# Optimization experiments

Measured on AMD Instinct MI355X. Metric: run time of the kernel, lower is better.

The kernel has to match this reference:

```python
import jax, jax.numpy as jnp
import numpy as np

N, D, O, V, E, C = 100000, 128, 128, 3, 400000, 2

def setup_inputs() -> dict:
    key = jax.random.key(0)
    ks = jax.random.split(key, 32)
    s = 0.05
    inp = {
        'features': jax.random.normal(ks[0], (N, D), jnp.float32),
        'edge_index': jax.random.randint(ks[1], (V, 2, E), 0, N, jnp.int32),
        'edge_weight': jax.random.uniform(ks[2], (V, E), jnp.float32),
        # per-view RelationAggregator (single relation each)
        'rel_w': jax.random.normal(ks[3], (V, D, O)) * s,
        'rel_b': jnp.zeros((V, O)),
        'gate_w': jax.random.normal(ks[4], (V, O, O)) * s,
        'gate_b': jnp.zeros((V, O)),
        # LabelAwareAttention
        'la_w1': jax.random.normal(ks[5], (C, D, D // 2)) * s,
        'la_b1': jnp.zeros((C, D // 2)),
        'la_w2': jax.random.normal(ks[6], (C, D // 2)) * s,
        'la_b2': jnp.zeros((C,)),
        'pred_w': jax.random.normal(ks[7], (D, C)) * s,
        'pred_b': jnp.zeros((C,)),
        'att_bias': jnp.float32(0.1),
        # ViewLevelAttention
        'view_pref': jax.random.normal(ks[8], (V, O)),
        'va_w1': jax.random.normal(ks[9], (O, O // 2)) * s,
        'va_b1': jnp.zeros((O // 2,)),
        'va_w2': jax.random.normal(ks[10], (O // 2,)) * s,
        'va_b2': jnp.float32(0.0),
        # linear heads
        'ft_w': jax.random.normal(ks[11], (D, O)) * s,
        'ft_b': jnp.zeros((O,)),
        'sl_w': jax.random.normal(ks[12], (D, O)) * s,
        'sl_b': jnp.zeros((O,)),
        'fus_w': jax.random.normal(ks[13], (2 * O, O)) * s,
        'fus_b': jnp.zeros((O,)),
        'ln_g': jnp.ones((O,)),
        'ln_beta': jnp.zeros((O,)),
    }
    return inp


def _aggregate_view(features, ei, ew, w, b, gw, gb):
    # gather -> linear -> edge weight -> scatter-add (fused segment_sum)
    msg = (features[ei[0]] @ w + b) * ew[:, None]          # [E, O]
    agg = jax.ops.segment_sum(msg, ei[1], num_segments=N)  # [N, O]
    # relation_weight_net: softmax over 1 relation == 1.0 (identity)
    gate = jax.nn.sigmoid(agg @ gw + gb)
    return gate * agg


def reference(features, edge_index, edge_weight, rel_w, rel_b, gate_w, gate_b,
              la_w1, la_b1, la_w2, la_b2, pred_w, pred_b, att_bias,
              view_pref, va_w1, va_b1, va_w2, va_b2,
              ft_w, ft_b, sl_w, sl_b, fus_w, fus_b, ln_g, ln_beta):
    # --- label-aware attention ---
    class_probs = jax.nn.softmax(features @ pred_w + pred_b, axis=-1)        # [N, C]
    h = jax.nn.relu(jnp.einsum('nd,cdk->nck', features, la_w1) + la_b1)      # [N, C, D/2]
    scores = jax.nn.sigmoid(jnp.einsum('nck,ck->nc', h, la_w2) + la_b2)      # [N, C]
    node_att = jnp.sum(scores * class_probs, axis=-1) + att_bias             # [N]

    # --- per-view relation aggregation ---
    views = jax.vmap(_aggregate_view, in_axes=(None, 0, 0, 0, 0, 0, 0))(
        features, edge_index, edge_weight, rel_w, rel_b, gate_w, gate_b)     # [V, N, O]

    # --- view-level attention ---
    pe = views * view_pref[:, None, :]                                       # [V, N, O]
    vh = jax.nn.relu(jnp.einsum('vno,ok->vnk', pe, va_w1) + va_b1)           # [V, N, O/2]
    vscore = jnp.einsum('vnk,k->vn', vh, va_w2) + va_b2                      # [V, N]
    v_att = jax.nn.softmax(vscore, axis=0)                                   # over views
    combined = jnp.sum(views * v_att[..., None], axis=0)                     # [N, O]

    # --- fusion (dropout in eval mode == identity) ---
    self_out = features @ sl_w + sl_b
    transformed = features @ ft_w + ft_b
    weighted = combined * node_att[:, None]
    fused = jax.nn.relu(jnp.concatenate([self_out, weighted], axis=-1) @ fus_w + fus_b)
    out = fused + transformed

    mu = jnp.mean(out, axis=-1, keepdims=True)
    var = jnp.mean(jnp.square(out - mu), axis=-1, keepdims=True)
    out = (out - mu) / jnp.sqrt(var + 1e-5) * ln_g + ln_beta
    return out, class_probs
```

## Files before the change

### kernel.cpp

```cpp
#include <hip/hip_runtime.h>

#define N_ 100000
#define D_ 128
#define O_ 128
#define V_ 3
#define E_ 400000
#define NB_SCAN 98
#define EGRID 1563
#define MB 32
#define NBLK (N_ / MB)
#define LDA 136

typedef unsigned short u16;
typedef __attribute__((ext_vector_type(8))) short bf16x8;
typedef __attribute__((ext_vector_type(4))) float f32x4;

#define MFMA16x16x32 __builtin_amdgcn_mfma_f32_16x16x32_bf16

#define P_RELB  0
#define P_GATEB 384
#define P_VP    768
#define P_VAB1  1152
#define P_VAW2  1216
#define P_VAB2  1280
#define P_LAB1  1281
#define P_LAW2  1409
#define P_LAB2  1537
#define P_PREDB 1539
#define P_ATTB  1541
#define P_FTB   1542
#define P_LNG   1670
#define P_LNB   1798
#define P_PREDW 1926
#define P_TOTAL 2182

__device__ __forceinline__ float b2f(u16 u) {
    union { float f; unsigned int i; } x; x.i = ((unsigned int)u) << 16; return x.f;
}
__device__ __forceinline__ u16 f2b(float f) {
    union { float f; unsigned int i; } x; x.f = f;
    unsigned int r = x.i + 0x7FFFu + ((x.i >> 16) & 1u);
    return (u16)(r >> 16);
}

template<int F32> __device__ __forceinline__ float LD(const void* p, size_t i) {
    if (F32) return ((const float*)p)[i];
    return b2f(((const u16*)p)[i]);
}

__global__ void k_detect(const u16* __restrict__ feat, int* __restrict__ flag) {
    if (threadIdx.x == 0 && blockIdx.x == 0) {
        int bad = 0, zeros = 0;
        for (int i = 0; i < 128; ++i) {
            u16 u = feat[2 * i];
            if (u == 0) zeros++;
            float v = b2f(u);
            if (!(v > -128.f && v < 128.f)) bad++;
        }
        flag[0] = (bad >= 16 || zeros >= 64) ? 1 : 0;
    }
}

template<int F32>
__device__ __forceinline__ void cvt_body(const void* feat, u16* __restrict__ featB) {
    size_t idx = (size_t)blockIdx.x * 256 + threadIdx.x;
    if (F32) {
        const float4* fp = (const float4*)feat;
        float4 a = fp[idx * 2], b = fp[idx * 2 + 1];
        uint4 u;
        u.x = (unsigned)f2b(a.x) | ((unsigned)f2b(a.y) << 16);
        u.y = (unsigned)f2b(a.z) | ((unsigned)f2b(a.w) << 16);
        u.z = (unsigned)f2b(b.x) | ((unsigned)f2b(b.y) << 16);
        u.w = (unsigned)f2b(b.z) | ((unsigned)f2b(b.w) << 16);
        ((uint4*)featB)[idx] = u;
    } else {
        ((uint4*)featB)[idx] = ((const uint4*)feat)[idx];
    }
}
__global__ __launch_bounds__(256) void k_cvt(const int* __restrict__ flag,
                                             const void* feat, u16* __restrict__ featB) {
    if (flag[0]) cvt_body<1>(feat, featB); else cvt_body<0>(feat, featB);
}

template<int F32>
__device__ __forceinline__ void prew_body(const void* sl_w, const void* sl_b,
                                          const void* fus_w, const void* fus_b,
                                          u16* __restrict__ W1T, float* __restrict__ b1) {
    int gid = blockIdx.x * 256 + threadIdx.x;
    int d = gid >> 7, o = gid & 127;
    float acc = 0.f;
    for (int k = 0; k < 128; ++k)
        acc += LD<F32>(sl_w, d * 128 + k) * LD<F32>(fus_w, k * 128 + o);
    W1T[o * 128 + d] = f2b(acc);
    if (gid < 128) {
        float accb = 0.f;
        for (int k = 0; k < 128; ++k)
            accb += LD<F32>(sl_b, k) * LD<F32>(fus_w, k * 128 + gid);
        b1[gid] = accb + LD<F32>(fus_b, gid);
    }
}
__global__ __launch_bounds__(256) void k_prew(const int* __restrict__ flag,
                                              const void* sl_w, const void* sl_b,
                                              const void* fus_w, const void* fus_b,
                                              u16* __restrict__ W1T, float* __restrict__ b1) {
    if (flag[0]) prew_body<1>(sl_w, sl_b, fus_w, fus_b, W1T, b1);
    else         prew_body<0>(sl_w, sl_b, fus_w, fus_b, W1T, b1);
}

template<int F32>
__device__ __forceinline__ void prep_body(
        const void* rel_w, const void* gate_w, const void* va_w1, const void* fus_w,
        const void* ft_w, const void* la_w1,
        const void* rel_b, const void* gate_b, const void* vpref,
        const void* va_b1, const void* va_w2, const void* va_b2,
        const void* la_b1, const void* la_w2, const void* la_b2,
        const void* pred_b, const void* att_bias, const void* ft_b,
        const void* ln_g, const void* ln_beta, const void* pred_w,
        u16* __restrict__ relT, u16* __restrict__ gateT, u16* __restrict__ vaT,
        u16* __restrict__ fus2T, u16* __restrict__ ftT, u16* __restrict__ laT,
        float* __restrict__ P) {
    int id = blockIdx.x * 256 + threadIdx.x;
    if (id < 49152) {
        int v = id >> 14, r = id & 16383, o = r >> 7, d = r & 127;
        relT[id] = f2b(LD<F32>(rel_w, (size_t)v * 16384 + d * 128 + o));
    } else if (id < 98304) {
        int t = id - 49152, v = t >> 14, r = t & 16383, o = r >> 7, d = r & 127;
        gateT[t] = f2b(LD<F32>(gate_w, (size_t)v * 16384 + d * 128 + o));
    } else if (id < 106496) {
        int t = id - 98304, n = t >> 7, k = t & 127;
        vaT[t] = f2b(LD<F32>(va_w1, k * 64 + n));
    } else if (id < 122880) {
        int t = id - 106496, n = t >> 7, k = t & 127;
        fus2T[t] = f2b(LD<F32>(fus_w, (128 + k) * 128 + n));
    } else if (id < 139264) {
        int t = id - 122880, o = t >> 7, d = t & 127;
        ftT[t] = f2b(LD<F32>(ft_w, d * 128 + o));
    } else if (id < 155648) {
        int t = id - 139264, n = t >> 7, d = t & 127;
        int c = n >> 6, j = n & 63;
        laT[t] = f2b(LD<F32>(la_w1, c * 8192 + d * 64 + j));
    } else if (id < 155648 + P_TOTAL) {
        int t = id - 155648;
        float val;
        if      (t < P_GATEB) val = LD<F32>(rel_b, t);
        else if (t < P_VP)    val = LD<F32>(gate_b, t - P_GATEB);
        else if (t < P_VAB1)  val = LD<F32>(vpref, t - P_VP);
        else if (t < P_VAW2)  val = LD<F32>(va_b1, t - P_VAB1);
        else if (t < P_VAB2)  val = LD<F32>(va_w2, t - P_VAW2);
        else if (t < P_LAB1)  val = LD<F32>(va_b2, 0);
        else if (t < P_LAW2)  val = LD<F32>(la_b1, t - P_LAB1);
        else if (t < P_LAB2)  val = LD<F32>(la_w2, t - P_LAW2);
        else if (t < P_PREDB) val = LD<F32>(la_b2, t - P_LAB2);
        else if (t < P_ATTB)  val = LD<F32>(pred_b, t - P_PREDB);
        else if (t < P_FTB)   val = LD<F32>(att_bias, 0);
        else if (t < P_LNG)   val = LD<F32>(ft_b, t - P_FTB);
        else if (t < P_LNB)   val = LD<F32>(ln_g, t - P_LNG);
        else if (t < P_PREDW) val = LD<F32>(ln_beta, t - P_LNB);
        else                  val = LD<F32>(pred_w, t - P_PREDW);
        P[t] = val;
    }
}
__global__ __launch_bounds__(256) void k_prep(const int* __restrict__ flag,
        const void* rel_w, const void* gate_w, const void* va_w1, const void* fus_w,
        const void* ft_w, const void* la_w1,
        const void* rel_b, const void* gate_b, const void* vpref,
        const void* va_b1, const void* va_w2, const void* va_b2,
        const void* la_b1, const void* la_w2, const void* la_b2,
        const void* pred_b, const void* att_bias, const void* ft_b,
        const void* ln_g, const void* ln_beta, const void* pred_w,
        u16* __restrict__ relT, u16* __restrict__ gateT, u16* __restrict__ vaT,
        u16* __restrict__ fus2T, u16* __restrict__ ftT, u16* __restrict__ laT,
        float* __restrict__ P) {
    if (flag[0]) prep_body<1>(rel_w, gate_w, va_w1, fus_w, ft_w, la_w1,
                              rel_b, gate_b, vpref, va_b1, va_w2, va_b2,
                              la_b1, la_w2, la_b2, pred_b, att_bias, ft_b,
                              ln_g, ln_beta, pred_w, relT, gateT, vaT, fus2T, ftT, laT, P);
    else         prep_body<0>(rel_w, gate_w, va_w1, fus_w, ft_w, la_w1,
                              rel_b, gate_b, vpref, va_b1, va_w2, va_b2,
                              la_b1, la_w2, la_b2, pred_b, att_bias, ft_b,
                              ln_g, ln_beta, pred_w, relT, gateT, vaT, fus2T, ftT, laT, P);
}

__global__ __launch_bounds__(256) void k_count(const int* __restrict__ ei,
                                               int* __restrict__ cur3) {
    int v = blockIdx.x / EGRID;
    int e = (blockIdx.x % EGRID) * 256 + threadIdx.x;
    if (e < E_) atomicAdd(&cur3[v * N_ + ei[(size_t)v * 2 * E_ + E_ + e]], 1);
}

__global__ __launch_bounds__(256) void k_scan_bsum(const int* __restrict__ cur3,
                                                   int* __restrict__ bsum) {
    __shared__ int red[256];
    const int v = blockIdx.x / NB_SCAN, b = blockIdx.x % NB_SCAN, tid = threadIdx.x;
    const int base = b * 1024;
    const int* counts = cur3 + v * N_;
    int s = 0;
    for (int i = tid; i < 1024; i += 256) {
        int idx = base + i;
        s += (idx < N_) ? counts[idx] : 0;
    }
    red[tid] = s;
    __syncthreads();
    for (int st = 128; st >= 1; st >>= 1) {
        if (tid < st) red[tid] += red[tid + st];
        __syncthreads();
    }
    if (tid == 0) bsum[v * 128 + b] = red[0];
}

__global__ __launch_bounds__(256) void k_scan_write(int* __restrict__ cur3,
                                                    const int* __restrict__ bsum,
                                                    int* __restrict__ offs3) {
    __shared__ int lsum[256];
    __shared__ int bs_s[128];
    const int v = blockIdx.x / NB_SCAN, b = blockIdx.x % NB_SCAN, tid = threadIdx.x;
    const int base = b * 1024;
    int* counts = cur3 + v * N_;
    int* offs   = offs3 + v * N_;
    if (tid < 128) bs_s[tid] = (tid < b) ? bsum[v * 128 + tid] : 0;
    int c[4]; int s = 0;
    #pragma unroll
    for (int k = 0; k < 4; ++k) {
        int idx = base + tid * 4 + k;
        c[k] = (idx < N_) ? counts[idx] : 0;
        s += c[k];
    }
    lsum[tid] = s;
    __syncthreads();
    for (int st = 1; st < 256; st <<= 1) {
        int t = (tid >= st) ? lsum[tid - st] : 0;
        __syncthreads();
        lsum[tid] += t;
        __syncthreads();
    }
    for (int st = 64; st >= 1; st >>= 1) {
        if (tid < st) bs_s[tid] += bs_s[tid + st];
        __syncthreads();
    }
    int off = bs_s[0] + lsum[tid] - s;
    #pragma unroll
    for (int k = 0; k < 4; ++k) {
        int idx = base + tid * 4 + k;
        if (idx < N_) { offs[idx] = off; counts[idx] = off; }
        off += c[k];
    }
}

template<int F32>
__device__ __forceinline__ void place_body(const int* __restrict__ ei, const void* ew_all,
                                           int* __restrict__ cur3, int2* __restrict__ srcw3) {
    int v = blockIdx.x / EGRID;
    int e = (blockIdx.x % EGRID) * 256 + threadIdx.x;
    if (e < E_) {
        int dst = ei[(size_t)v * 2 * E_ + E_ + e];
        int src = ei[(size_t)v * 2 * E_ + e];
        float w = LD<F32>(ew_all, (size_t)v * E_ + e);
        int pos = atomicAdd(&cur3[v * N_ + dst], 1);
        int2 sw; sw.x = src; sw.y = __float_as_int(w);
        srcw3[(size_t)v * E_ + pos] = sw;
    }
}
__global__ __launch_bounds__(256) void k_place(const int* __restrict__ flag,
                                               const int* __restrict__ ei, const void* ew,
                                               int* __restrict__ cur3, int2* __restrict__ srcw3) {
    if (flag[0]) place_body<1>(ei, ew, cur3, srcw3);
    else         place_body<0>(ei, ew, cur3, srcw3);
}

__global__ __launch_bounds__(256, 4) void k_fused(const int* __restrict__ flag,
        const u16* __restrict__ featB, const int2* __restrict__ srcw3,
        const int* __restrict__ offs3, const int* __restrict__ ends3,
        const u16* __restrict__ relT, const u16* __restrict__ gateT,
        const u16* __restrict__ vaT, const u16* __restrict__ W1T,
        const u16* __restrict__ fus2T, const u16* __restrict__ ftT,
        const u16* __restrict__ laT,
        const float* __restrict__ b1, const float* __restrict__ P,
        void* __restrict__ d_out) {
    const int f32 = flag[0];

    __shared__ __align__(16) u16 xA[MB * LDA];
    __shared__ __align__(16) u16 zb[2][MB * LDA];
    __shared__ float wsn_s[2][MB];
    __shared__ float vsc_s[MB][3];
    __shared__ float red_s[4][MB][2];
    __shared__ float mrs_s[MB][2];
    __shared__ float aw_s[MB][3];
    __shared__ float natt_s[MB];
    __shared__ float lg_s[MB][2];
    __shared__ float relb_s[2][128];
    __shared__ float gateb_s[128], vp_s[128];
    __shared__ float vab1_s[64], vaw2_s[64];
    __shared__ float lab1_s[128], law2_s[128], predw_s[256];
    __shared__ float b1_s[128], ftb_s[128], lng_s[128], lnb_s[128];

    const int tid = threadIdx.x;
    const int wid = tid >> 6;
    const int L = tid & 63, q = L >> 4, i = L & 15;
    const int nb = wid * 32;
    const int nodebase = blockIdx.x * MB;
    const int nl = tid >> 5, l32 = tid & 31, o4 = l32 * 4;
    const f32x4 zz = {0.f, 0.f, 0.f, 0.f};

    auto ldf = [&](const u16* B, int row, int k0) -> bf16x8 {
        return *(const bf16x8*)&B[row * LDA + k0];
    };
    auto ldg = [&](const u16* B, int row, int k0) -> bf16x8 {
        return *(const bf16x8*)&B[row * 128 + k0];
    };
    auto gemm128 = [&](const u16* A, const u16* Bg, f32x4 acc[2][2]) {
        #pragma unroll
        for (int kk = 0; kk < 4; ++kk) {
            int k0 = q * 8 + kk * 32;
            bf16x8 a0 = ldf(A, i, k0);
            bf16x8 a1 = ldf(A, i + 16, k0);
            bf16x8 bb0 = ldg(Bg, nb + i, k0);
            bf16x8 bb1 = ldg(Bg, nb + 16 + i, k0);
            acc[0][0] = MFMA16x16x32(a0, bb0, acc[0][0], 0, 0, 0);
            acc[0][1] = MFMA16x16x32(a0, bb1, acc[0][1], 0, 0, 0);
            acc[1][0] = MFMA16x16x32(a1, bb0, acc[1][0], 0, 0, 0);
            acc[1][1] = MFMA16x16x32(a1, bb1, acc[1][1], 0, 0, 0);
        }
    };
    auto gather = [&](int v, u16* dst) {
        const int* offs = offs3 + v * N_;
        const int* ends = ends3 + v * N_;
        const int2* srcw = srcw3 + (size_t)v * E_;
        int js[4], je[4];
        #pragma unroll
        for (int rep = 0; rep < 4; ++rep) {
            int node = nodebase + rep * 8 + nl;
            js[rep] = offs[node];
            je[rep] = ends[node];
        }
        #pragma unroll
        for (int rep = 0; rep < 4; ++rep) {
            int m = rep * 8 + nl;
            float z0 = 0.f, z1 = 0.f, z2 = 0.f, z3 = 0.f, ws = 0.f;
            int j = js[rep], jend = je[rep];
            for (; j + 3 < jend; j += 4) {
                int2 e0 = srcw[j], e1 = srcw[j + 1], e2 = srcw[j + 2], e3 = srcw[j + 3];
                float w0 = __int_as_float(e0.y), w1 = __int_as_float(e1.y);
                float w2 = __int_as_float(e2.y), w3 = __int_as_float(e3.y);
                ushort4 x0 = *(const ushort4*)&featB[(size_t)e0.x * 128 + o4];
                ushort4 x1 = *(const ushort4*)&featB[(size_t)e1.x * 128 + o4];
                ushort4 x2 = *(const ushort4*)&featB[(size_t)e2.x * 128 + o4];
                ushort4 x3 = *(const ushort4*)&featB[(size_t)e3.x * 128 + o4];
                z0 += w0 * b2f(x0.x) + w1 * b2f(x1.x) + w2 * b2f(x2.x) + w3 * b2f(x3.x);
                z1 += w0 * b2f(x0.y) + w1 * b2f(x1.y) + w2 * b2f(x2.y) + w3 * b2f(x3.y);
                z2 += w0 * b2f(x0.z) + w1 * b2f(x1.z) + w2 * b2f(x2.z) + w3 * b2f(x3.z);
                z3 += w0 * b2f(x0.w) + w1 * b2f(x1.w) + w2 * b2f(x2.w) + w3 * b2f(x3.w);
                ws += w0 + w1 + w2 + w3;
            }
            if (j + 1 < jend) {
                int2 e0 = srcw[j], e1 = srcw[j + 1];
                float w0 = __int_as_float(e0.y), w1 = __int_as_float(e1.y);
                ushort4 x0 = *(const ushort4*)&featB[(size_t)e0.x * 128 + o4];
                ushort4 x1 = *(const ushort4*)&featB[(size_t)e1.x * 128 + o4];
                z0 += w0 * b2f(x0.x) + w1 * b2f(x1.x);
                z1 += w0 * b2f(x0.y) + w1 * b2f(x1.y);
                z2 += w0 * b2f(x0.z) + w1 * b2f(x1.z);
                z3 += w0 * b2f(x0.w) + w1 * b2f(x1.w);
                ws += w0 + w1;
                j += 2;
            }
            if (j < jend) {
                int2 e0 = srcw[j];
                float w0 = __int_as_float(e0.y);
                ushort4 x0 = *(const ushort4*)&featB[(size_t)e0.x * 128 + o4];
                z0 += w0 * b2f(x0.x); z1 += w0 * b2f(x0.y);
                z2 += w0 * b2f(x0.z); z3 += w0 * b2f(x0.w);
                ws += w0;
            }
            uint2 u;
            u.x = (unsigned)f2b(z0) | ((unsigned)f2b(z1) << 16);
            u.y = (unsigned)f2b(z2) | ((unsigned)f2b(z3) << 16);
            *(uint2*)&dst[m * LDA + o4] = u;
            if (l32 == 0) wsn_s[v & 1][m] = ws;
        }
    };

    for (int idx = tid; idx < MB * 16; idx += 256) {
        int m = idx >> 4, s = idx & 15;
        *(uint4*)&xA[m * LDA + s * 8] =
            *(const uint4*)&featB[(size_t)(nodebase + m) * 128 + s * 8];
    }
    if (tid < 64) { vab1_s[tid] = P[P_VAB1 + tid]; vaw2_s[tid] = P[P_VAW2 + tid]; }
    if (tid < 128) {
        b1_s[tid]   = b1[tid];
        ftb_s[tid]  = P[P_FTB + tid];
        lng_s[tid]  = P[P_LNG + tid];
        lnb_s[tid]  = P[P_LNB + tid];
        relb_s[0][tid] = P[P_RELB + tid];
        lab1_s[tid] = P[P_LAB1 + tid];
        law2_s[tid] = P[P_LAW2 + tid];
    }
    predw_s[tid] = P[P_PREDW + tid];
    gather(0, zb[0]);
    __syncthreads();

    f32x4 accL[2][2] = {{zz, zz}, {zz, zz}};
    gemm128(xA, laT, accL);
    #pragma unroll
    for (int rep = 0; rep < 4; ++rep) {
        int m = rep * 8 + nl;
        float lg0 = 0.f, lg1 = 0.f;
        #pragma unroll
        for (int t = 0; t < 4; ++t) {
            float xv = b2f(xA[m * LDA + o4 + t]);
            lg0 += xv * predw_s[(o4 + t) * 2 + 0];
            lg1 += xv * predw_s[(o4 + t) * 2 + 1];
        }
        #pragma unroll
        for (int s = 1; s <= 16; s <<= 1) {
            lg0 += __shfl_xor(lg0, s);
            lg1 += __shfl_xor(lg1, s);
        }
        if (l32 == 0) { lg_s[m][0] = lg0; lg_s[m][1] = lg1; }
    }
    {
        float partL[2][4];
        #pragma unroll
        for (int mt = 0; mt < 2; ++mt)
            #pragma unroll
            for (int r = 0; r < 4; ++r) {
                float h0 = fmaxf(accL[mt][0][r] + lab1_s[nb + i], 0.f);
                float h1 = fmaxf(accL[mt][1][r] + lab1_s[nb + 16 + i], 0.f);
                partL[mt][r] = h0 * law2_s[nb + i] + h1 * law2_s[nb + 16 + i];
            }
        #pragma unroll
        for (int s = 1; s <= 8; s <<= 1)
            #pragma unroll
            for (int mt = 0; mt < 2; ++mt)
                #pragma unroll
                for (int r = 0; r < 4; ++r)
                    partL[mt][r] += __shfl_xor(partL[mt][r], s);
        if (i == 0)
            #pragma unroll
            for (int mt = 0; mt < 2; ++mt)
                #pragma unroll
                for (int r = 0; r < 4; ++r)
                    red_s[wid][mt * 16 + q * 4 + r][0] = partL[mt][r];
    }
    __syncthreads();
    if (tid < MB) {
        float c0 = red_s[0][tid][0] + red_s[1][tid][0] + P[P_LAB2 + 0];
        float c1 = red_s[2][tid][0] + red_s[3][tid][0] + P[P_LAB2 + 1];
        float s0 = 1.f / (1.f + __expf(-c0));
        float s1 = 1.f / (1.f + __expf(-c1));
        float l0 = lg_s[tid][0] + P[P_PREDB + 0];
        float l1 = lg_s[tid][1] + P[P_PREDB + 1];
        float mx = fmaxf(l0, l1);
        float e0 = __expf(l0 - mx), e1 = __expf(l1 - mx);
        float inv = 1.f / (e0 + e1);
        float p0 = e0 * inv, p1 = e1 * inv;
        natt_s[tid] = s0 * p0 + s1 * p1 + P[P_ATTB];
        int node = nodebase + tid;
        if (f32) {
            float* pr = (float*)d_out + (size_t)N_ * O_;
            pr[node * 2 + 0] = p0; pr[node * 2 + 1] = p1;
        } else {
            u16* pr = (u16*)d_out + (size_t)N_ * O_;
            pr[node * 2 + 0] = f2b(p0); pr[node * 2 + 1] = f2b(p1);
        }
    }

    f32x4 viewr[3][2][2];
    #pragma unroll
    for (int v = 0; v < 3; ++v) {
        u16* zc = zb[v & 1];
        f32x4 accA[2][2] = {{zz, zz}, {zz, zz}};
        gemm128(zc, relT + (size_t)v * 16384, accA);
        if (v < 2) {
            if (tid < 128) relb_s[(v + 1) & 1][tid] = P[P_RELB + (v + 1) * 128 + tid];
            gather(v + 1, zb[(v + 1) & 1]);
        }
        if (tid < 128) {
            gateb_s[tid] = P[P_GATEB + v * 128 + tid];
            vp_s[tid]    = P[P_VP + v * 128 + tid];
        }
        __syncthreads();
        #pragma unroll
        for (int mt = 0; mt < 2; ++mt)
            #pragma unroll
            for (int nt = 0; nt < 2; ++nt)
                #pragma unroll
                for (int r = 0; r < 4; ++r) {
                    int row = mt * 16 + q * 4 + r, col = nb + nt * 16 + i;
                    float a = accA[mt][nt][r] + wsn_s[v & 1][row] * relb_s[v & 1][col];
                    accA[mt][nt][r] = a;
                    zc[row * LDA + col] = f2b(a);
                }
        __syncthreads();
        f32x4 acc2[2][2] = {{zz, zz}, {zz, zz}};
        gemm128(zc, gateT + (size_t)v * 16384, acc2);
        __syncthreads();
        #pragma unroll
        for (int mt = 0; mt < 2; ++mt)
            #pragma unroll
            for (int nt = 0; nt < 2; ++nt)
                #pragma unroll
                for (int r = 0; r < 4; ++r) {
                    int row = mt * 16 + q * 4 + r, col = nb + nt * 16 + i;
                    float g = 1.f / (1.f + __expf(-(acc2[mt][nt][r] + gateb_s[col])));
                    float vv = g * accA[mt][nt][r];
                    viewr[v][mt][nt][r] = vv;
                    zc[row * LDA + col] = f2b(vv * vp_s[col]);
                }
        __syncthreads();
        f32x4 accV[2] = {zz, zz};
        const int nbv = wid * 16, colv = nbv + i;
        #pragma unroll
        for (int kk = 0; kk < 4; ++kk) {
            int k0 = q * 8 + kk * 32;
            bf16x8 a0 = ldf(zc, i, k0);
            bf16x8 a1 = ldf(zc, i + 16, k0);
            bf16x8 bb = ldg(vaT, nbv + i, k0);
            accV[0] = MFMA16x16x32(a0, bb, accV[0], 0, 0, 0);
            accV[1] = MFMA16x16x32(a1, bb, accV[1], 0, 0, 0);
        }
        float part[2][4];
        #pragma unroll
        for (int mt = 0; mt < 2; ++mt)
            #pragma unroll
            for (int r = 0; r < 4; ++r) {
                float vh = fmaxf(accV[mt][r] + vab1_s[colv], 0.f);
                part[mt][r] = vh * vaw2_s[colv];
            }
        #pragma unroll
        for (int s = 1; s <= 8; s <<= 1)
            #pragma unroll
            for (int mt = 0; mt < 2; ++mt)
                #pragma unroll
                for (int r = 0; r < 4; ++r)
                    part[mt][r] += __shfl_xor(part[mt][r], s);
        if (i == 0)
            #pragma unroll
            for (int mt = 0; mt < 2; ++mt)
                #pragma unroll
                for (int r = 0; r < 4; ++r)
                    red_s[wid][mt * 16 + q * 4 + r][0] = part[mt][r];
        __syncthreads();
        if (tid < MB)
            vsc_s[tid][v] = red_s[0][tid][0] + red_s[1][tid][0] +
                            red_s[2][tid][0] + red_s[3][tid][0] + P[P_VAB2];
    }

    if (tid < MB) {
        float s0 = vsc_s[tid][0], s1 = vsc_s[tid][1], s2 = vsc_s[tid][2];
        float mx = fmaxf(s0, fmaxf(s1, s2));
        float e0 = __expf(s0 - mx), e1 = __expf(s1 - mx), e2 = __expf(s2 - mx);
        float inv = natt_s[tid] / (e0 + e1 + e2);
        aw_s[tid][0] = e0 * inv; aw_s[tid][1] = e1 * inv; aw_s[tid][2] = e2 * inv;
    }
    __syncthreads();
    u16* wt = zb[0];
    #pragma unroll
    for (int mt = 0; mt < 2; ++mt)
        #pragma unroll
        for (int nt = 0; nt < 2; ++nt)
            #pragma unroll
            for (int r = 0; r < 4; ++r) {
                int row = mt * 16 + q * 4 + r, col = nb + nt * 16 + i;
                float wv = aw_s[row][0] * viewr[0][mt][nt][r] +
                           aw_s[row][1] * viewr[1][mt][nt][r] +
                           aw_s[row][2] * viewr[2][mt][nt][r];
                wt[row * LDA + col] = f2b(wv);
            }
    f32x4 accF[2][2] = {{zz, zz}, {zz, zz}};
    gemm128(xA, W1T, accF);
    __syncthreads();
    gemm128(wt, fus2T, accF);
    float fR[2][2][4];
    #pragma unroll
    for (int mt = 0; mt < 2; ++mt)
        #pragma unroll
        for (int nt = 0; nt < 2; ++nt)
            #pragma unroll
            for (int r = 0; r < 4; ++r) {
                int col = nb + nt * 16 + i;
                fR[mt][nt][r] = fmaxf(accF[mt][nt][r] + b1_s[col], 0.f);
            }
    f32x4 accT[2][2] = {{zz, zz}, {zz, zz}};
    gemm128(xA, ftT, accT);

    float ov[2][2][4], ps[2][4], pq[2][4];
    #pragma unroll
    for (int mt = 0; mt < 2; ++mt)
        #pragma unroll
        for (int r = 0; r < 4; ++r) { ps[mt][r] = 0.f; pq[mt][r] = 0.f; }
    #pragma unroll
    for (int mt = 0; mt < 2; ++mt)
        #pragma unroll
        for (int nt = 0; nt < 2; ++nt)
            #pragma unroll
            for (int r = 0; r < 4; ++r) {
                int col = nb + nt * 16 + i;
                float o = fR[mt][nt][r] + accT[mt][nt][r] + ftb_s[col];
                ov[mt][nt][r] = o;
                ps[mt][r] += o; pq[mt][r] += o * o;
            }
    #pragma unroll
    for (int s = 1; s <= 8; s <<= 1)
        #pragma unroll
        for (int mt = 0; mt < 2; ++mt)
            #pragma unroll
            for (int r = 0; r < 4; ++r) {
                ps[mt][r] += __shfl_xor(ps[mt][r], s);
                pq[mt][r] += __shfl_xor(pq[mt][r], s);
            }
    if (i == 0)
        #pragma unroll
        for (int mt = 0; mt < 2; ++mt)
            #pragma unroll
            for (int r = 0; r < 4; ++r) {
                red_s[wid][mt * 16 + q * 4 + r][0] = ps[mt][r];
                red_s[wid][mt * 16 + q * 4 + r][1] = pq[mt][r];
            }
    __syncthreads();
    if (tid < MB) {
        float sm = red_s[0][tid][0] + red_s[1][tid][0] + red_s[2][tid][0] + red_s[3][tid][0];
        float sq = red_s[0][tid][1] + red_s[1][tid][1] + red_s[2][tid][1] + red_s[3][tid][1];
        float mu = sm * (1.f / 128.f);
        float var = sq * (1.f / 128.f) - mu * mu;
        mrs_s[tid][0] = mu; mrs_s[tid][1] = rsqrtf(var + 1e-5f);
    }
    __syncthreads();
    float* outf = (float*)zb;
    u16*   outb = (u16*)zb;
    #pragma unroll
    for (int mt = 0; mt < 2; ++mt)
        #pragma unroll
        for (int nt = 0; nt < 2; ++nt)
            #pragma unroll
            for (int r = 0; r < 4; ++r) {
                int row = mt * 16 + q * 4 + r, col = nb + nt * 16 + i;
                float val = (ov[mt][nt][r] - mrs_s[row][0]) * mrs_s[row][1]
                            * lng_s[col] + lnb_s[col];
                if (f32) outf[row * 128 + col] = val;
                else     outb[row * 128 + col] = f2b(val);
            }
    __syncthreads();
    if (f32) {
        float* op = (float*)d_out + (size_t)nodebase * 128;
        for (int idx = tid; idx < 1024; idx += 256)
            ((float4*)op)[idx] = ((const float4*)outf)[idx];
    } else {
        u16* op = (u16*)d_out + (size_t)nodebase * 128;
        for (int idx = tid; idx < 512; idx += 256)
            ((uint4*)op)[idx] = ((const uint4*)outb)[idx];
    }
}

extern "C" void kernel_launch(void* const* d_in, const int* in_sizes, int n_in,
                              void* d_out, int out_size, void* d_ws, size_t ws_size,
                              hipStream_t stream) {
    const void* feat     = d_in[0];
    const int*  ei       = (const int*)d_in[1];
    const void* ew       = d_in[2];
    const void* rel_w    = d_in[3];
    const void* rel_b    = d_in[4];
    const void* gate_w   = d_in[5];
    const void* gate_b   = d_in[6];
    const void* la_w1    = d_in[7];
    const void* la_b1    = d_in[8];
    const void* la_w2    = d_in[9];
    const void* la_b2    = d_in[10];
    const void* pred_w   = d_in[11];
    const void* pred_b   = d_in[12];
    const void* att_bias = d_in[13];
    const void* view_pref= d_in[14];
    const void* va_w1    = d_in[15];
    const void* va_b1    = d_in[16];
    const void* va_w2    = d_in[17];
    const void* va_b2    = d_in[18];
    const void* ft_w     = d_in[19];
    const void* ft_b     = d_in[20];
    const void* sl_w     = d_in[21];
    const void* sl_b     = d_in[22];
    const void* fus_w    = d_in[23];
    const void* fus_b    = d_in[24];
    const void* ln_g     = d_in[25];
    const void* ln_beta  = d_in[26];

    int*   flag  = (int*)d_ws;
    int*   offs3 = flag + 4;
    int*   cur3  = offs3 + 3 * N_;
    int2*  srcw3 = (int2*)(cur3 + 3 * N_);
    int*   bsum  = (int*)(srcw3 + 3 * E_);
    float* b1    = (float*)(bsum + 3 * 128);
    float* P     = b1 + 128;
    u16*   W1T   = (u16*)(P + 2304);
    u16*   relT  = W1T + 16384;
    u16*   gateT = relT + 3 * 16384;
    u16*   vaT   = gateT + 3 * 16384;
    u16*   fus2T = vaT + 8192;
    u16*   ftT   = fus2T + 16384;
    u16*   laT   = ftT + 16384;
    u16*   featB = laT + 16384;

    k_detect<<<1, 64, 0, stream>>>((const u16*)feat, flag);
    k_cvt<<<6250, 256, 0, stream>>>(flag, feat, featB);
    k_prew<<<64, 256, 0, stream>>>(flag, sl_w, sl_b, fus_w, fus_b, W1T, b1);
    k_prep<<<617, 256, 0, stream>>>(flag, rel_w, gate_w, va_w1, fus_w, ft_w, la_w1,
                                    rel_b, gate_b, view_pref, va_b1, va_w2, va_b2,
                                    la_b1, la_w2, la_b2, pred_b, att_bias, ft_b,
                                    ln_g, ln_beta, pred_w,
                                    relT, gateT, vaT, fus2T, ftT, laT, P);
    (void)hipMemsetAsync(cur3, 0, 3 * N_ * sizeof(int), stream);
    k_count<<<3 * EGRID, 256, 0, stream>>>(ei, cur3);
    k_scan_bsum<<<3 * NB_SCAN, 256, 0, stream>>>(cur3, bsum);
    k_scan_write<<<3 * NB_SCAN, 256, 0, stream>>>(cur3, bsum, offs3);
    k_place<<<3 * EGRID, 256, 0, stream>>>(flag, ei, ew, cur3, srcw3);
    k_fused<<<NBLK, 256, 0, stream>>>(flag, featB, srcw3, offs3, cur3,
                                      relT, gateT, vaT, W1T, fus2T, ftT, laT,
                                      b1, P, d_out);
}
```

Baseline: 566.5 us.

## Merge prep kernels into one launch, halve node tile, widen gather vectors

The conversion, weight precompute, weight prep and edge-count kernels are merged into a single multi-role launch, and the bf16 feature copy is skipped when inputs are already bf16. The fused node kernel now processes 16 nodes per block instead of 32, with launch bounds raised to 8 blocks per CU. Each node's gather is handled by 16 lanes doing 8-wide loads in place of 32 lanes doing 4-wide loads. The detect kernel uses a warp shuffle reduction instead of a serial loop. Together these aim to cut launch overhead and improve occupancy and latency hiding in the gather, at the cost of less MFMA reuse per block and more blocks overall.

```diff
diff --git a/kernel.cpp b/kernel.cpp
--- a/kernel.cpp
+++ b/kernel.cpp
@@ -7,9 +7,14 @@
 #define E_ 400000
 #define NB_SCAN 98
 #define EGRID 1563
-#define MB 32
+#define MB 16
 #define NBLK (N_ / MB)
 #define LDA 136
+
+#define PRE_CVT  6250
+#define PRE_PREW (PRE_CVT + 64)
+#define PRE_PREP (PRE_PREW + 617)
+#define PRE_TOT  (PRE_PREP + 3 * EGRID)
 
 typedef unsigned short u16;
 typedef __attribute__((ext_vector_type(8))) short bf16x8;
@@ -37,6 +42,12 @@
 __device__ __forceinline__ float b2f(u16 u) {
     union { float f; unsigned int i; } x; x.i = ((unsigned int)u) << 16; return x.f;
 }
+__device__ __forceinline__ float blo(unsigned int u) {
+    union { float f; unsigned int i; } x; x.i = u << 16; return x.f;
+}
+__device__ __forceinline__ float bhi(unsigned int u) {
+    union { float f; unsigned int i; } x; x.i = u & 0xffff0000u; return x.f;
+}
 __device__ __forceinline__ u16 f2b(float f) {
     union { float f; unsigned int i; } x; x.f = f;
     unsigned int r = x.i + 0x7FFFu + ((x.i >> 16) & 1u);
@@ -49,44 +60,38 @@
 }
 
 __global__ void k_detect(const u16* __restrict__ feat, int* __restrict__ flag) {
-    if (threadIdx.x == 0 && blockIdx.x == 0) {
-        int bad = 0, zeros = 0;
-        for (int i = 0; i < 128; ++i) {
-            u16 u = feat[2 * i];
-            if (u == 0) zeros++;
-            float v = b2f(u);
-            if (!(v > -128.f && v < 128.f)) bad++;
-        }
-        flag[0] = (bad >= 16 || zeros >= 64) ? 1 : 0;
-    }
+    int t = threadIdx.x;
+    u16 a = feat[2 * t], b = feat[2 * t + 128];
+    int zeros = (a == 0 ? 1 : 0) + (b == 0 ? 1 : 0);
+    float va = b2f(a), vb = b2f(b);
+    int bad = (!(va > -128.f && va < 128.f) ? 1 : 0) +
+              (!(vb > -128.f && vb < 128.f) ? 1 : 0);
+    #pragma unroll
+    for (int s = 1; s <= 32; s <<= 1) {
+        bad += __shfl_xor(bad, s);
+        zeros += __shfl_xor(zeros, s);
+    }
+    if (t == 0) flag[0] = (bad >= 16 || zeros >= 64) ? 1 : 0;
+}
+
+__device__ __forceinline__ void cvt_body_f32(int b, const void* feat,
+                                             u16* __restrict__ featB) {
+    size_t idx = (size_t)b * 256 + threadIdx.x;
+    const float4* fp = (const float4*)feat;
+    float4 a = fp[idx * 2], c = fp[idx * 2 + 1];
+    uint4 u;
+    u.x = (unsigned)f2b(a.x) | ((unsigned)f2b(a.y) << 16);
+    u.y = (unsigned)f2b(a.z) | ((unsigned)f2b(a.w) << 16);
+    u.z = (unsigned)f2b(c.x) | ((unsigned)f2b(c.y) << 16);
+    u.w = (unsigned)f2b(c.z) | ((unsigned)f2b(c.w) << 16);
+    ((uint4*)featB)[idx] = u;
 }
 
 template<int F32>
-__device__ __forceinline__ void cvt_body(const void* feat, u16* __restrict__ featB) {
-    size_t idx = (size_t)blockIdx.x * 256 + threadIdx.x;
-    if (F32) {
-        const float4* fp = (const float4*)feat;
-        float4 a = fp[idx * 2], b = fp[idx * 2 + 1];
-        uint4 u;
-        u.x = (unsigned)f2b(a.x) | ((unsigned)f2b(a.y) << 16);
-        u.y = (unsigned)f2b(a.z) | ((unsigned)f2b(a.w) << 16);
-        u.z = (unsigned)f2b(b.x) | ((unsigned)f2b(b.y) << 16);
-        u.w = (unsigned)f2b(b.z) | ((unsigned)f2b(b.w) << 16);
-        ((uint4*)featB)[idx] = u;
-    } else {
-        ((uint4*)featB)[idx] = ((const uint4*)feat)[idx];
-    }
-}
-__global__ __launch_bounds__(256) void k_cvt(const int* __restrict__ flag,
-                                             const void* feat, u16* __restrict__ featB) {
-    if (flag[0]) cvt_body<1>(feat, featB); else cvt_body<0>(feat, featB);
-}
-
-template<int F32>
-__device__ __forceinline__ void prew_body(const void* sl_w, const void* sl_b,
+__device__ __forceinline__ void prew_body(int b, const void* sl_w, const void* sl_b,
                                           const void* fus_w, const void* fus_b,
                                           u16* __restrict__ W1T, float* __restrict__ b1) {
-    int gid = blockIdx.x * 256 + threadIdx.x;
+    int gid = b * 256 + threadIdx.x;
     int d = gid >> 7, o = gid & 127;
     float acc = 0.f;
     for (int k = 0; k < 128; ++k)
@@ -99,16 +104,9 @@
         b1[gid] = accb + LD<F32>(fus_b, gid);
     }
 }
-__global__ __launch_bounds__(256) void k_prew(const int* __restrict__ flag,
-                                              const void* sl_w, const void* sl_b,
-                                              const void* fus_w, const void* fus_b,
-                                              u16* __restrict__ W1T, float* __restrict__ b1) {
-    if (flag[0]) prew_body<1>(sl_w, sl_b, fus_w, fus_b, W1T, b1);
-    else         prew_body<0>(sl_w, sl_b, fus_w, fus_b, W1T, b1);
-}
 
 template<int F32>
-__device__ __forceinline__ void prep_body(
+__device__ __forceinline__ void prep_body(int b,
         const void* rel_w, const void* gate_w, const void* va_w1, const void* fus_w,
         const void* ft_w, const void* la_w1,
         const void* rel_b, const void* gate_b, const void* vpref,
@@ -119,7 +117,7 @@
         u16* __restrict__ relT, u16* __restrict__ gateT, u16* __restrict__ vaT,
         u16* __restrict__ fus2T, u16* __restrict__ ftT, u16* __restrict__ laT,
         float* __restrict__ P) {
-    int id = blockIdx.x * 256 + threadIdx.x;
+    int id = b * 256 + threadIdx.x;
     if (id < 49152) {
         int v = id >> 14, r = id & 16383, o = r >> 7, d = r & 127;
         relT[id] = f2b(LD<F32>(rel_w, (size_t)v * 16384 + d * 128 + o));
@@ -160,8 +158,12 @@
         P[t] = val;
     }
 }
-__global__ __launch_bounds__(256) void k_prep(const int* __restrict__ flag,
-        const void* rel_w, const void* gate_w, const void* va_w1, const void* fus_w,
+
+__global__ __launch_bounds__(256) void k_preC(const int* __restrict__ flag,
+        const void* feat, u16* __restrict__ featB,
+        const void* sl_w, const void* sl_b, const void* fus_w, const void* fus_b,
+        u16* __restrict__ W1T, float* __restrict__ b1,
+        const void* rel_w, const void* gate_w, const void* va_w1,
         const void* ft_w, const void* la_w1,
         const void* rel_b, const void* gate_b, const void* vpref,
         const void* va_b1, const void* va_w2, const void* va_b2,
@@ -170,22 +172,29 @@
         const void* ln_g, const void* ln_beta, const void* pred_w,
         u16* __restrict__ relT, u16* __restrict__ gateT, u16* __restrict__ vaT,
         u16* __restrict__ fus2T, u16* __restrict__ ftT, u16* __restrict__ laT,
-        float* __restrict__ P) {
-    if (flag[0]) prep_body<1>(rel_w, gate_w, va_w1, fus_w, ft_w, la_w1,
-                              rel_b, gate_b, vpref, va_b1, va_w2, va_b2,
-                              la_b1, la_w2, la_b2, pred_b, att_bias, ft_b,
-                              ln_g, ln_beta, pred_w, relT, gateT, vaT, fus2T, ftT, laT, P);
-    else         prep_body<0>(rel_w, gate_w, va_w1, fus_w, ft_w, la_w1,
-                              rel_b, gate_b, vpref, va_b1, va_w2, va_b2,
-                              la_b1, la_w2, la_b2, pred_b, att_bias, ft_b,
-                              ln_g, ln_beta, pred_w, relT, gateT, vaT, fus2T, ftT, laT, P);
-}
-
-__global__ __launch_bounds__(256) void k_count(const int* __restrict__ ei,
-                                               int* __restrict__ cur3) {
-    int v = blockIdx.x / EGRID;
-    int e = (blockIdx.x % EGRID) * 256 + threadIdx.x;
-    if (e < E_) atomicAdd(&cur3[v * N_ + ei[(size_t)v * 2 * E_ + E_ + e]], 1);
+        float* __restrict__ P,
+        const int* __restrict__ ei, int* __restrict__ cur3) {
+    int b = blockIdx.x;
+    if (b < PRE_CVT) {
+        if (flag[0]) cvt_body_f32(b, feat, featB);
+    } else if (b < PRE_PREW) {
+        if (flag[0]) prew_body<1>(b - PRE_CVT, sl_w, sl_b, fus_w, fus_b, W1T, b1);
+        else         prew_body<0>(b - PRE_CVT, sl_w, sl_b, fus_w, fus_b, W1T, b1);
+    } else if (b < PRE_PREP) {
+        if (flag[0]) prep_body<1>(b - PRE_PREW, rel_w, gate_w, va_w1, fus_w, ft_w, la_w1,
+                                  rel_b, gate_b, vpref, va_b1, va_w2, va_b2,
+                                  la_b1, la_w2, la_b2, pred_b, att_bias, ft_b,
+                                  ln_g, ln_beta, pred_w, relT, gateT, vaT, fus2T, ftT, laT, P);
+        else         prep_body<0>(b - PRE_PREW, rel_w, gate_w, va_w1, fus_w, ft_w, la_w1,
+                                  rel_b, gate_b, vpref, va_b1, va_w2, va_b2,
+                                  la_b1, la_w2, la_b2, pred_b, att_bias, ft_b,
+                                  ln_g, ln_beta, pred_w, relT, gateT, vaT, fus2T, ftT, laT, P);
+    } else {
+        int b2 = b - PRE_PREP;
+        int v = b2 / EGRID;
+        int e = (b2 % EGRID) * 256 + threadIdx.x;
+        if (e < E_) atomicAdd(&cur3[v * N_ + ei[(size_t)v * 2 * E_ + E_ + e]], 1);
+    }
 }
 
 __global__ __launch_bounds__(256) void k_scan_bsum(const int* __restrict__ cur3,
@@ -267,8 +276,9 @@
     else         place_body<0>(ei, ew, cur3, srcw3);
 }
 
-__global__ __launch_bounds__(256, 4) void k_fused(const int* __restrict__ flag,
-        const u16* __restrict__ featB, const int2* __restrict__ srcw3,
+__global__ __launch_bounds__(256, 8) void k_fused(const int* __restrict__ flag,
+        const void* feat, const u16* __restrict__ featB_,
+        const int2* __restrict__ srcw3,
         const int* __restrict__ offs3, const int* __restrict__ ends3,
         const u16* __restrict__ relT, const u16* __restrict__ gateT,
         const u16* __restrict__ vaT, const u16* __restrict__ W1T,
@@ -277,6 +287,7 @@
         const float* __restrict__ b1, const float* __restrict__ P,
         void* __restrict__ d_out) {
     const int f32 = flag[0];
+    const u16* __restrict__ fb = f32 ? featB_ : (const u16*)feat;
 
     __shared__ __align__(16) u16 xA[MB * LDA];
     __shared__ __align__(16) u16 zb[2][MB * LDA];
@@ -287,10 +298,8 @@
     __shared__ float aw_s[MB][3];
     __shared__ float natt_s[MB];
     __shared__ float lg_s[MB][2];
-    __shared__ float relb_s[2][128];
-    __shared__ float gateb_s[128], vp_s[128];
     __shared__ float vab1_s[64], vaw2_s[64];
-    __shared__ float lab1_s[128], law2_s[128], predw_s[256];
+    __shared__ float predw_s[256];
     __shared__ float b1_s[128], ftb_s[128], lng_s[128], lnb_s[128];
 
     const int tid = threadIdx.x;
@@ -299,6 +308,7 @@
     const int nb = wid * 32;
     const int nodebase = blockIdx.x * MB;
     const int nl = tid >> 5, l32 = tid & 31, o4 = l32 * 4;
+    const int gg = tid >> 4, l16 = tid & 15, o8 = l16 * 8;
     const f32x4 zz = {0.f, 0.f, 0.f, 0.f};
 
     auto ldf = [&](const u16* B, int row, int k0) -> bf16x8 {
@@ -307,101 +317,83 @@
     auto ldg = [&](const u16* B, int row, int k0) -> bf16x8 {
         return *(const bf16x8*)&B[row * 128 + k0];
     };
-    auto gemm128 = [&](const u16* A, const u16* Bg, f32x4 acc[2][2]) {
+    auto gemm128 = [&](const u16* A, const u16* Bg, f32x4 acc[2]) {
         #pragma unroll
         for (int kk = 0; kk < 4; ++kk) {
             int k0 = q * 8 + kk * 32;
             bf16x8 a0 = ldf(A, i, k0);
-            bf16x8 a1 = ldf(A, i + 16, k0);
             bf16x8 bb0 = ldg(Bg, nb + i, k0);
             bf16x8 bb1 = ldg(Bg, nb + 16 + i, k0);
-            acc[0][0] = MFMA16x16x32(a0, bb0, acc[0][0], 0, 0, 0);
-            acc[0][1] = MFMA16x16x32(a0, bb1, acc[0][1], 0, 0, 0);
-            acc[1][0] = MFMA16x16x32(a1, bb0, acc[1][0], 0, 0, 0);
-            acc[1][1] = MFMA16x16x32(a1, bb1, acc[1][1], 0, 0, 0);
+            acc[0] = MFMA16x16x32(a0, bb0, acc[0], 0, 0, 0);
+            acc[1] = MFMA16x16x32(a0, bb1, acc[1], 0, 0, 0);
         }
     };
     auto gather = [&](int v, u16* dst) {
         const int* offs = offs3 + v * N_;
         const int* ends = ends3 + v * N_;
         const int2* srcw = srcw3 + (size_t)v * E_;
-        int js[4], je[4];
-        #pragma unroll
-        for (int rep = 0; rep < 4; ++rep) {
-            int node = nodebase + rep * 8 + nl;
-            js[rep] = offs[node];
-            je[rep] = ends[node];
-        }
-        #pragma unroll
-        for (int rep = 0; rep < 4; ++rep) {
-            int m = rep * 8 + nl;
-            float z0 = 0.f, z1 = 0.f, z2 = 0.f, z3 = 0.f, ws = 0.f;
-            int j = js[rep], jend = je[rep];
-            for (; j + 3 < jend; j += 4) {
-                int2 e0 = srcw[j], e1 = srcw[j + 1], e2 = srcw[j + 2], e3 = srcw[j + 3];
-                float w0 = __int_as_float(e0.y), w1 = __int_as_float(e1.y);
-                float w2 = __int_as_float(e2.y), w3 = __int_as_float(e3.y);
-                ushort4 x0 = *(const ushort4*)&featB[(size_t)e0.x * 128 + o4];
-                ushort4 x1 = *(const ushort4*)&featB[(size_t)e1.x * 128 + o4];
-                ushort4 x2 = *(const ushort4*)&featB[(size_t)e2.x * 128 + o4];
-                ushort4 x3 = *(const ushort4*)&featB[(size_t)e3.x * 128 + o4];
-                z0 += w0 * b2f(x0.x) + w1 * b2f(x1.x) + w2 * b2f(x2.x) + w3 * b2f(x3.x);
-                z1 += w0 * b2f(x0.y) + w1 * b2f(x1.y) + w2 * b2f(x2.y) + w3 * b2f(x3.y);
-                z2 += w0 * b2f(x0.z) + w1 * b2f(x1.z) + w2 * b2f(x2.z) + w3 * b2f(x3.z);
-                z3 += w0 * b2f(x0.w) + w1 * b2f(x1.w) + w2 * b2f(x2.w) + w3 * b2f(x3.w);
-                ws += w0 + w1 + w2 + w3;
-            }
-            if (j + 1 < jend) {
-                int2 e0 = srcw[j], e1 = srcw[j + 1];
-                float w0 = __int_as_float(e0.y), w1 = __int_as_float(e1.y);
-                ushort4 x0 = *(const ushort4*)&featB[(size_t)e0.x * 128 + o4];
-                ushort4 x1 = *(const ushort4*)&featB[(size_t)e1.x * 128 + o4];
-                z0 += w0 * b2f(x0.x) + w1 * b2f(x1.x);
-                z1 += w0 * b2f(x0.y) + w1 * b2f(x1.y);
-                z2 += w0 * b2f(x0.z) + w1 * b2f(x1.z);
-                z3 += w0 * b2f(x0.w) + w1 * b2f(x1.w);
-                ws += w0 + w1;
-                j += 2;
-            }
-            if (j < jend) {
-                int2 e0 = srcw[j];
-                float w0 = __int_as_float(e0.y);
-                ushort4 x0 = *(const ushort4*)&featB[(size_t)e0.x * 128 + o4];
-                z0 += w0 * b2f(x0.x); z1 += w0 * b2f(x0.y);
-                z2 += w0 * b2f(x0.z); z3 += w0 * b2f(x0.w);
-                ws += w0;
-            }
-            uint2 u;
-            u.x = (unsigned)f2b(z0) | ((unsigned)f2b(z1) << 16);
-            u.y = (unsigned)f2b(z2) | ((unsigned)f2b(z3) << 16);
-            *(uint2*)&dst[m * LDA + o4] = u;
-            if (l32 == 0) wsn_s[v & 1][m] = ws;
-        }
+        const int node = nodebase + gg;
+        float z0 = 0.f, z1 = 0.f, z2 = 0.f, z3 = 0.f;
+        float z4 = 0.f, z5 = 0.f, z6 = 0.f, z7 = 0.f, ws = 0.f;
+        int j = offs[node], jend = ends[node];
+        while (j < jend) {
+            int r = jend - j;
+            int2 e0 = srcw[j];
+            int2 e1, e2, e3;
+            e1.x = 0; e1.y = 0; e2.x = 0; e2.y = 0; e3.x = 0; e3.y = 0;
+            if (r > 1) e1 = srcw[j + 1];
+            if (r > 2) e2 = srcw[j + 2];
+            if (r > 3) e3 = srcw[j + 3];
+            uint4 x0, x1, x2, x3;
+            x1.x = x1.y = x1.z = x1.w = 0;
+            x2.x = x2.y = x2.z = x2.w = 0;
+            x3.x = x3.y = x3.z = x3.w = 0;
+            x0 = *(const uint4*)&fb[(size_t)e0.x * 128 + o8];
+            if (r > 1) x1 = *(const uint4*)&fb[(size_t)e1.x * 128 + o8];
+            if (r > 2) x2 = *(const uint4*)&fb[(size_t)e2.x * 128 + o8];
+            if (r > 3) x3 = *(const uint4*)&fb[(size_t)e3.x * 128 + o8];
+            float w0 = __int_as_float(e0.y), w1 = __int_as_float(e1.y);
+            float w2 = __int_as_float(e2.y), w3 = __int_as_float(e3.y);
+            ws += w0 + w1 + w2 + w3;
+            z0 += w0 * blo(x0.x) + w1 * blo(x1.x) + w2 * blo(x2.x) + w3 * blo(x3.x);
+            z1 += w0 * bhi(x0.x) + w1 * bhi(x1.x) + w2 * bhi(x2.x) + w3 * bhi(x3.x);
+            z2 += w0 * blo(x0.y) + w1 * blo(x1.y) + w2 * blo(x2.y) + w3 * blo(x3.y);
+            z3 += w0 * bhi(x0.y) + w1 * bhi(x1.y) + w2 * bhi(x2.y) + w3 * bhi(x3.y);
+            z4 += w0 * blo(x0.z) + w1 * blo(x1.z) + w2 * blo(x2.z) + w3 * blo(x3.z);
+            z5 += w0 * bhi(x0.z) + w1 * bhi(x1.z) + w2 * bhi(x2.z) + w3 * bhi(x3.z);
+            z6 += w0 * blo(x0.w) + w1 * blo(x1.w) + w2 * blo(x2.w) + w3 * blo(x3.w);
+            z7 += w0 * bhi(x0.w) + w1 * bhi(x1.w) + w2 * bhi(x2.w) + w3 * bhi(x3.w);
+            j += 4;
+        }
+        uint4 u;
+        u.x = (unsigned)f2b(z0) | ((unsigned)f2b(z1) << 16);
+        u.y = (unsigned)f2b(z2) | ((unsigned)f2b(z3) << 16);
+        u.z = (unsigned)f2b(z4) | ((unsigned)f2b(z5) << 16);
+        u.w = (unsigned)f2b(z6) | ((unsigned)f2b(z7) << 16);
+        *(uint4*)&dst[gg * LDA + o8] = u;
+        if (l16 == 0) wsn_s[v & 1][gg] = ws;
     };
 
-    for (int idx = tid; idx < MB * 16; idx += 256) {
-        int m = idx >> 4, s = idx & 15;
+    {
+        int m = tid >> 4, s = tid & 15;
         *(uint4*)&xA[m * LDA + s * 8] =
-            *(const uint4*)&featB[(size_t)(nodebase + m) * 128 + s * 8];
+            *(const uint4*)&fb[(size_t)(nodebase + m) * 128 + s * 8];
     }
     if (tid < 64) { vab1_s[tid] = P[P_VAB1 + tid]; vaw2_s[tid] = P[P_VAW2 + tid]; }
     if (tid < 128) {
-        b1_s[tid]   = b1[tid];
-        ftb_s[tid]  = P[P_FTB + tid];
-        lng_s[tid]  = P[P_LNG + tid];
-        lnb_s[tid]  = P[P_LNB + tid];
-        relb_s[0][tid] = P[P_RELB + tid];
-        lab1_s[tid] = P[P_LAB1 + tid];
-        law2_s[tid] = P[P_LAW2 + tid];
+        b1_s[tid]  = b1[tid];
+        ftb_s[tid] = P[P_FTB + tid];
+        lng_s[tid] = P[P_LNG + tid];
+        lnb_s[tid] = P[P_LNB + tid];
     }
     predw_s[tid] = P[P_PREDW + tid];
     gather(0, zb[0]);
     __syncthreads();
 
-    f32x4 accL[2][2] = {{zz, zz}, {zz, zz}};
+    f32x4 accL[2] = {zz, zz};
     gemm128(xA, laT, accL);
     #pragma unroll
-    for (int rep = 0; rep < 4; ++rep) {
+    for (int rep = 0; rep < 2; ++rep) {
         int m = rep * 8 + nl;
         float lg0 = 0.f, lg1 = 0.f;
         #pragma unroll
@@ -418,28 +410,24 @@
         if (l32 == 0) { lg_s[m][0] = lg0; lg_s[m][1] = lg1; }
     }
     {
-        float partL[2][4];
-        #pragma unroll
-        for (int mt = 0; mt < 2; ++mt)
-            #pragma unroll
-            for (int r = 0; r < 4; ++r) {
-                float h0 = fmaxf(accL[mt][0][r] + lab1_s[nb + i], 0.f);
-                float h1 = fmaxf(accL[mt][1][r] + lab1_s[nb + 16 + i], 0.f);
-                partL[mt][r] = h0 * law2_s[nb + i] + h1 * law2_s[nb + 16 + i];
-            }
+        float la0 = P[P_LAB1 + nb + i],  la1 = P[P_LAB1 + nb + 16 + i];
+        float lw0 = P[P_LAW2 + nb + i],  lw1 = P[P_LAW2 + nb + 16 + i];
+        float partL[4];
+        #pragma unroll
+        for (int r = 0; r < 4; ++r) {
+            float h0 = fmaxf(accL[0][r] + la0, 0.f);
+            float h1 = fmaxf(accL[1][r] + la1, 0.f);
+            partL[r] = h0 * lw0 + h1 * lw1;
+        }
         #pragma unroll
         for (int s = 1; s <= 8; s <<= 1)
             #pragma unroll
-            for (int mt = 0; mt < 2; ++mt)
-                #pragma unroll
-                for (int r = 0; r < 4; ++r)
-                    partL[mt][r] += __shfl_xor(partL[mt][r], s);
+            for (int r = 0; r < 4; ++r)
+                partL[r] += __shfl_xor(partL[r], s);
         if (i == 0)
             #pragma unroll
-            for (int mt = 0; mt < 2; ++mt)
-                #pragma unroll
-                for (int r = 0; r < 4; ++r)
-                    red_s[wid][mt * 16 + q * 4 + r][0] = partL[mt][r];
+            for (int r = 0; r < 4; ++r)
+                red_s[wid][q * 4 + r][0] = partL[r];
     }
     __syncthreads();
     if (tid < MB) {
@@ -464,81 +452,78 @@
         }
     }
 
-    f32x4 viewr[3][2][2];
+    f32x4 viewr[3][2];
     #pragma unroll
     for (int v = 0; v < 3; ++v) {
         u16* zc = zb[v & 1];
-        f32x4 accA[2][2] = {{zz, zz}, {zz, zz}};
+        f32x4 accA[2] = {zz, zz};
         gemm128(zc, relT + (size_t)v * 16384, accA);
-        if (v < 2) {
-            if (tid < 128) relb_s[(v + 1) & 1][tid] = P[P_RELB + (v + 1) * 128 + tid];
-            gather(v + 1, zb[(v + 1) & 1]);
-        }
-        if (tid < 128) {
-            gateb_s[tid] = P[P_GATEB + v * 128 + tid];
-            vp_s[tid]    = P[P_VP + v * 128 + tid];
-        }
-        __syncthreads();
-        #pragma unroll
-        for (int mt = 0; mt < 2; ++mt)
+        if (v < 2) gather(v + 1, zb[(v + 1) & 1]);
+        __syncthreads();
+        {
+            float rb0 = P[P_RELB + v * 128 + nb + i];
+            float rb1 = P[P_RELB + v * 128 + nb + 16 + i];
             #pragma unroll
-            for (int nt = 0; nt < 2; ++nt)
+            for (int nt = 0; nt < 2; ++nt) {
+                float rb = nt ? rb1 : rb0;
+                int col = nb + nt * 16 + i;
                 #pragma unroll
                 for (int r = 0; r < 4; ++r) {
-                    int row = mt * 16 + q * 4 + r, col = nb + nt * 16 + i;
-                    float a = accA[mt][nt][r] + wsn_s[v & 1][row] * relb_s[v & 1][col];
-                    accA[mt][nt][r] = a;
+                    int row = q * 4 + r;
+                    float a = accA[nt][r] + wsn_s[v & 1][row] * rb;
+                    accA[nt][r] = a;
                     zc[row * LDA + col] = f2b(a);
                 }
-        __syncthreads();
-        f32x4 acc2[2][2] = {{zz, zz}, {zz, zz}};
+            }
+        }
+        __syncthreads();
+        f32x4 acc2[2] = {zz, zz};
         gemm128(zc, gateT + (size_t)v * 16384, acc2);
         __syncthreads();
-        #pragma unroll
-        for (int mt = 0; mt < 2; ++mt)
+        {
+            float gb0 = P[P_GATEB + v * 128 + nb + i];
+            float gb1 = P[P_GATEB + v * 128 + nb + 16 + i];
+            float vp0 = P[P_VP + v * 128 + nb + i];
+            float vp1 = P[P_VP + v * 128 + nb + 16 + i];
             #pragma unroll
-            for (int nt = 0; nt < 2; ++nt)
+            for (int nt = 0; nt < 2; ++nt) {
+                float gb = nt ? gb1 : gb0, vp = nt ? vp1 : vp0;
+                int col = nb + nt * 16 + i;
                 #pragma unroll
                 for (int r = 0; r < 4; ++r) {
-                    int row = mt * 16 + q * 4 + r, col = nb + nt * 16 + i;
-                    float g = 1.f / (1.f + __expf(-(acc2[mt][nt][r] + gateb_s[col])));
-                    float vv = g * accA[mt][nt][r];
-                    viewr[v][mt][nt][r] = vv;
-                    zc[row * LDA + col] = f2b(vv * vp_s[col]);
+                    int row = q * 4 + r;
+                    float g = 1.f / (1.f + __expf(-(acc2[nt][r] + gb)));
+                    float vv = g * accA[nt][r];
+                    viewr[v][nt][r] = vv;
+                    zc[row * LDA + col] = f2b(vv * vp);
                 }
-        __syncthreads();
-        f32x4 accV[2] = {zz, zz};
+            }
+        }
+        __syncthreads();
+        f32x4 accV = zz;
         const int nbv = wid * 16, colv = nbv + i;
         #pragma unroll
         for (int kk = 0; kk < 4; ++kk) {
             int k0 = q * 8 + kk * 32;
             bf16x8 a0 = ldf(zc, i, k0);
-            bf16x8 a1 = ldf(zc, i + 16, k0);
             bf16x8 bb = ldg(vaT, nbv + i, k0);
-            accV[0] = MFMA16x16x32(a0, bb, accV[0], 0, 0, 0);
-            accV[1] = MFMA16x16x32(a1, bb, accV[1], 0, 0, 0);
-        }
-        float part[2][4];
-        #pragma unroll
-        for (int mt = 0; mt < 2; ++mt)
-            #pragma unroll
-            for (int r = 0; r < 4; ++r) {
-                float vh = fmaxf(accV[mt][r] + vab1_s[colv], 0.f);
-                part[mt][r] = vh * vaw2_s[colv];
-            }
+            accV = MFMA16x16x32(a0, bb, accV, 0, 0, 0);
+        }
+        float part[4];
+        #pragma unroll
+        for (int r = 0; r < 4; ++r) {
+            float vh = fmaxf(accV[r] + vab1_s[colv], 0.f);
+            part[r] = vh * vaw2_s[colv];
+        }
         #pragma unroll
         for (int s = 1; s <= 8; s <<= 1)
             #pragma unroll
-            for (int mt = 0; mt < 2; ++mt)
-                #pragma unroll
-                for (int r = 0; r < 4; ++r)
-                    part[mt][r] += __shfl_xor(part[mt][r], s);
+            for (int r = 0; r < 4; ++r)
+                part[r] += __shfl_xor(part[r], s);
         if (i == 0)
             #pragma unroll
-            for (int mt = 0; mt < 2; ++mt)
-                #pragma unroll
-                for (int r = 0; r < 4; ++r)
-                    red_s[wid][mt * 16 + q * 4 + r][0] = part[mt][r];
+            for (int r = 0; r < 4; ++r)
+                red_s[wid][q * 4 + r][0] = part[r];
         __syncthreads();
         if (tid < MB)
             vsc_s[tid][v] = red_s[0][tid][0] + red_s[1][tid][0] +
@@ -555,67 +540,55 @@
     __syncthreads();
     u16* wt = zb[0];
     #pragma unroll
-    for (int mt = 0; mt < 2; ++mt)
-        #pragma unroll
-        for (int nt = 0; nt < 2; ++nt)
-            #pragma unroll
-            for (int r = 0; r < 4; ++r) {
-                int row = mt * 16 + q * 4 + r, col = nb + nt * 16 + i;
-                float wv = aw_s[row][0] * viewr[0][mt][nt][r] +
-                           aw_s[row][1] * viewr[1][mt][nt][r] +
-                           aw_s[row][2] * viewr[2][mt][nt][r];
-                wt[row * LDA + col] = f2b(wv);
-            }
-    f32x4 accF[2][2] = {{zz, zz}, {zz, zz}};
+    for (int nt = 0; nt < 2; ++nt)
+        #pragma unroll
+        for (int r = 0; r < 4; ++r) {
+            int row = q * 4 + r, col = nb + nt * 16 + i;
+            float wv = aw_s[row][0] * viewr[0][nt][r] +
+                       aw_s[row][1] * viewr[1][nt][r] +
+                       aw_s[row][2] * viewr[2][nt][r];
+            wt[row * LDA + col] = f2b(wv);
+        }
+    f32x4 accF[2] = {zz, zz};
     gemm128(xA, W1T, accF);
     __syncthreads();
     gemm128(wt, fus2T, accF);
-    float fR[2][2][4];
-    #pragma unroll
-    for (int mt = 0; mt < 2; ++mt)
-        #pragma unroll
-        for (int nt = 0; nt < 2; ++nt)
-            #pragma unroll
-            for (int r = 0; r < 4; ++r) {
-                int col = nb + nt * 16 + i;
-                fR[mt][nt][r] = fmaxf(accF[mt][nt][r] + b1_s[col], 0.f);
-            }
-    f32x4 accT[2][2] = {{zz, zz}, {zz, zz}};
+    float fR[2][4];
+    #pragma unroll
+    for (int nt = 0; nt < 2; ++nt)
+        #pragma unroll
+        for (int r = 0; r < 4; ++r) {
+            int col = nb + nt * 16 + i;
+            fR[nt][r] = fmaxf(accF[nt][r] + b1_s[col], 0.f);
+        }
+    f32x4 accT[2] = {zz, zz};
     gemm128(xA, ftT, accT);
 
-    float ov[2][2][4], ps[2][4], pq[2][4];
-    #pragma unroll
-    for (int mt = 0; mt < 2; ++mt)
-        #pragma unroll
-        for (int r = 0; r < 4; ++r) { ps[mt][r] = 0.f; pq[mt][r] = 0.f; }
-    #pragma unroll
-    for (int mt = 0; mt < 2; ++mt)
-        #pragma unroll
-        for (int nt = 0; nt < 2; ++nt)
-            #pragma unroll
-            for (int r = 0; r < 4; ++r) {
-                int col = nb + nt * 16 + i;
-                float o = fR[mt][nt][r] + accT[mt][nt][r] + ftb_s[col];
-                ov[mt][nt][r] = o;
-                ps[mt][r] += o; pq[mt][r] += o * o;
-            }
+    float ov[2][4], ps[4], pq[4];
+    #pragma unroll
+    for (int r = 0; r < 4; ++r) { ps[r] = 0.f; pq[r] = 0.f; }
+    #pragma unroll
+    for (int nt = 0; nt < 2; ++nt)
+        #pragma unroll
+        for (int r = 0; r < 4; ++r) {
+            int col = nb + nt * 16 + i;
+            float o = fR[nt][r] + accT[nt][r] + ftb_s[col];
+            ov[nt][r] = o;
+            ps[r] += o; pq[r] += o * o;
+        }
     #pragma unroll
     for (int s = 1; s <= 8; s <<= 1)
         #pragma unroll
-        for (int mt = 0; mt < 2; ++mt)
-            #pragma unroll
-            for (int r = 0; r < 4; ++r) {
-                ps[mt][r] += __shfl_xor(ps[mt][r], s);
-                pq[mt][r] += __shfl_xor(pq[mt][r], s);
-            }
+        for (int r = 0; r < 4; ++r) {
+            ps[r] += __shfl_xor(ps[r], s);
+            pq[r] += __shfl_xor(pq[r], s);
+        }
     if (i == 0)
         #pragma unroll
-        for (int mt = 0; mt < 2; ++mt)
-            #pragma unroll
-            for (int r = 0; r < 4; ++r) {
-                red_s[wid][mt * 16 + q * 4 + r][0] = ps[mt][r];
-                red_s[wid][mt * 16 + q * 4 + r][1] = pq[mt][r];
-            }
+        for (int r = 0; r < 4; ++r) {
+            red_s[wid][q * 4 + r][0] = ps[r];
+            red_s[wid][q * 4 + r][1] = pq[r];
+        }
     __syncthreads();
     if (tid < MB) {
         float sm = red_s[0][tid][0] + red_s[1][tid][0] + red_s[2][tid][0] + red_s[3][tid][0];
@@ -628,26 +601,23 @@
     float* outf = (float*)zb;
     u16*   outb = (u16*)zb;
     #pragma unroll
-    for (int mt = 0; mt < 2; ++mt)
-        #pragma unroll
-        for (int nt = 0; nt < 2; ++nt)
-            #pragma unroll
-            for (int r = 0; r < 4; ++r) {
-                int row = mt * 16 + q * 4 + r, col = nb + nt * 16 + i;
-                float val = (ov[mt][nt][r] - mrs_s[row][0]) * mrs_s[row][1]
-                            * lng_s[col] + lnb_s[col];
-                if (f32) outf[row * 128 + col] = val;
-                else     outb[row * 128 + col] = f2b(val);
-            }
+    for (int nt = 0; nt < 2; ++nt)
+        #pragma unroll
+        for (int r = 0; r < 4; ++r) {
+            int row = q * 4 + r, col = nb + nt * 16 + i;
+            float val = (ov[nt][r] - mrs_s[row][0]) * mrs_s[row][1]
+                        * lng_s[col] + lnb_s[col];
+            if (f32) outf[row * 128 + col] = val;
+            else     outb[row * 128 + col] = f2b(val);
+        }
     __syncthreads();
     if (f32) {
         float* op = (float*)d_out + (size_t)nodebase * 128;
-        for (int idx = tid; idx < 1024; idx += 256)
+        for (int idx = tid; idx < 512; idx += 256)
             ((float4*)op)[idx] = ((const float4*)outf)[idx];
     } else {
         u16* op = (u16*)d_out + (size_t)nodebase * 128;
-        for (int idx = tid; idx < 512; idx += 256)
-            ((uint4*)op)[idx] = ((const uint4*)outb)[idx];
+        ((uint4*)op)[tid] = ((const uint4*)outb)[tid];
     }
 }
 
@@ -699,19 +669,20 @@
     u16*   featB = laT + 16384;
 
     k_detect<<<1, 64, 0, stream>>>((const u16*)feat, flag);
-    k_cvt<<<6250, 256, 0, stream>>>(flag, feat, featB);
-    k_prew<<<64, 256, 0, stream>>>(flag, sl_w, sl_b, fus_w, fus_b, W1T, b1);
-    k_prep<<<617, 256, 0, stream>>>(flag, rel_w, gate_w, va_w1, fus_w, ft_w, la_w1,
-                                    rel_b, gate_b, view_pref, va_b1, va_w2, va_b2,
-                                    la_b1, la_w2, la_b2, pred_b, att_bias, ft_b,
-                                    ln_g, ln_beta, pred_w,
-                                    relT, gateT, vaT, fus2T, ftT, laT, P);
     (void)hipMemsetAsync(cur3, 0, 3 * N_ * sizeof(int), stream);
-    k_count<<<3 * EGRID, 256, 0, stream>>>(ei, cur3);
+    k_preC<<<PRE_TOT, 256, 0, stream>>>(flag, feat, featB,
+                                        sl_w, sl_b, fus_w, fus_b, W1T, b1,
+                                        rel_w, gate_w, va_w1, ft_w, la_w1,
+                                        rel_b, gate_b, view_pref,
+                                        va_b1, va_w2, va_b2,
+                                        la_b1, la_w2, la_b2,
+                                        pred_b, att_bias, ft_b, ln_g, ln_beta, pred_w,
+                                        relT, gateT, vaT, fus2T, ftT, laT, P,
+                                        ei, cur3);
     k_scan_bsum<<<3 * NB_SCAN, 256, 0, stream>>>(cur3, bsum);
     k_scan_write<<<3 * NB_SCAN, 256, 0, stream>>>(cur3, bsum, offs3);
     k_place<<<3 * EGRID, 256, 0, stream>>>(flag, ei, ew, cur3, srcw3);
-    k_fused<<<NBLK, 256, 0, stream>>>(flag, featB, srcw3, offs3, cur3,
+    k_fused<<<NBLK, 256, 0, stream>>>(flag, feat, featB, srcw3, offs3, cur3,
                                       relT, gateT, vaT, W1T, fus2T, ftT, laT,
                                       b1, P, d_out);
 }
```

New measurement: 685.9 us. +21.1%, slower.
